# Kernel tuning notes

Measured on AMD Instinct MI355X. Metric: run time of the kernel, lower is better.

Reference implementation:

```python
import jax, jax.numpy as jnp
import numpy as np

# pywt db4 decomposition lowpass filter
DEC_LO = np.array([-0.010597401785069032, 0.0328830116668852, 0.030841381835560764,
                   -0.18703481171909309, -0.027983769416859854, 0.6308807679298589,
                   0.7148465705529157, 0.2303778133088965])
# pytorch_wavelets pre-reverses filters so that torch's cross-correlation conv1d
# implements true convolution; lax.conv_general_dilated is also cross-correlation,
# so we use the same reversed kernel.
KERNEL_LO = jnp.asarray(DEC_LO[::-1].copy(), dtype=jnp.float32)
FLEN = 8


def dwt_lo(x):
    # Single-level db4 lowpass analysis with 'zero' padding, matching
    # pytorch_wavelets afb1d (mode='zero'). x: [B, N, D] -> [B, (N+7)//2, D]
    B, N, D = x.shape
    out = (N + FLEN - 1) // 2            # pywt.dwt_coeff_len(N, 8, 'zero')
    p = 2 * (out - 1) - N + FLEN         # total zero padding
    xr = x.transpose(0, 2, 1).reshape(B * D, 1, N)
    y = jax.lax.conv_general_dilated(xr, KERNEL_LO[None, None, :],
                                     window_strides=(2,),
                                     padding=[(p // 2, p - p // 2)])
    return y.reshape(B, D, out).transpose(0, 2, 1)


def setup_inputs() -> dict:
    key = jax.random.key(0)
    k1, k2 = jax.random.split(key)
    x = jax.random.normal(k1, (32, 4097, 768), dtype=jnp.float32)
    cls_attention_map = jax.random.uniform(k2, (32, 4096), dtype=jnp.float32)
    return {"x": x, "cls_attention_map": cls_attention_map}


def reference(x, cls_attention_map):
    factors = jnp.array([1.5, 0.5], dtype=jnp.float32)  # sorted descending
    B, N, D = x.shape
    cls_tok, patches = x[:, :1], x[:, 1:]

    # per-sample entropy of the CLS attention map
    ent = -jnp.sum(cls_attention_map * jnp.log2(cls_attention_map + 1e-9), axis=-1)  # [B]
    mean, std = ent.mean(), ent.std(ddof=1)  # torch .std() is unbiased
    thr = mean - factors * std               # [2]
    lvl = jnp.sum(ent[:, None] < thr[None, :], axis=1)          # [B]
    lvl = jnp.where(std < 1e-6, jnp.ones_like(lvl), lvl)        # degenerate-std fallback
    lvl = jnp.clip(lvl, 1, factors.shape[0])                    # clamp_min_(1)

    # compute both experts densely, then per-sample select (replaces gather/scatter)
    y1 = dwt_lo(patches)   # level-1 Yl : [B, L1, D], L1 = 2051
    y2 = dwt_lo(y1)        # level-2 Yl : [B, L2, D], L2 = 1029 (cascaded lowpass = J=2 cA)
    L1, L2 = y1.shape[1], y2.shape[1]
    y2p = jnp.pad(y2, ((0, 0), (0, L1 - L2), (0, 0)))

    is1 = (lvl == 1)
    final_patches = jnp.where(is1[:, None, None], y1, y2p)      # [B, L1, D]
    out_len = jnp.where(is1, L1, L2)                            # [B]

    final_x = jnp.concatenate([cls_tok, final_patches], axis=1)  # [B, 1+L1, D]
    mask = jnp.arange(L1)[None, :] < out_len[:, None]
    mask = jnp.concatenate([jnp.ones((B, 1), dtype=bool), mask], axis=1)
    return final_x, mask
```

## Files before the change

### kernel.cpp

```cpp
#include <hip/hip_runtime.h>
#include <hip/hip_bf16.h>
#include <math.h>


typedef float f4 __attribute__((ext_vector_type(4)));

#define B_       32
#define NTOK     4097
#define NPATCH   4096
#define D_       768
#define D4_      192
#define L1_      2051
#define L2_      1029
#define OUTROWS  2052
#define TOUT     16
#define NTILES   129
#define NWG      (B_ * NTILES)

__device__ __constant__ float KLO[8] = {
     0.2303778133088965f,
     0.7148465705529157f,
     0.6308807679298589f,
    -0.027983769416859854f,
    -0.18703481171909309f,
     0.030841381835560764f,
     0.0328830116668852f,
    -0.010597401785069032f
};

__device__ __forceinline__ f4 dot8v(const f4 w[8]) {
    f4 a = KLO[0] * w[0];
#pragma unroll
    for (int t = 1; t < 8; ++t) {
        a.x = fmaf(KLO[t], w[t].x, a.x);
        a.y = fmaf(KLO[t], w[t].y, a.y);
        a.z = fmaf(KLO[t], w[t].z, a.z);
        a.w = fmaf(KLO[t], w[t].w, a.w);
    }
    return a;
}

__global__ void ent_kernel(const float* __restrict__ att, double* __restrict__ ent) {
    __shared__ double sm[256];
    const int b = blockIdx.x;
    const float* a = att + (size_t)b * NPATCH;
    double acc = 0.0;
    for (int i = threadIdx.x; i < NPATCH; i += 256) {
        double v = (double)a[i];
        acc += v * log2(v + 1e-9);
    }
    sm[threadIdx.x] = acc;
    __syncthreads();
    for (int s = 128; s > 0; s >>= 1) {
        if (threadIdx.x < s) sm[threadIdx.x] += sm[threadIdx.x + s];
        __syncthreads();
    }
    if (threadIdx.x == 0) ent[b] = -sm[0];
}

__global__ __launch_bounds__(192) void dwt_kernel(const f4* __restrict__ x,
                                                  const double* __restrict__ ent,
                                                  f4* __restrict__ out,
                                                  float* __restrict__ mask) {
    const int bid  = blockIdx.x;
    const int lid  = (bid & 7) * (NWG / 8) + (bid >> 3);
    const int b    = lid / NTILES;
    const int tile = lid % NTILES;
    const int o0   = tile * TOUT;
    const int d    = threadIdx.x;

    const f4* xb = x + (size_t)b * NTOK * D4_ + d;
    f4* ob = out + (size_t)b * OUTROWS * D4_ + d;

    const f4 z4 = (f4)(0.0f);
    auto xload = [&](int q) -> f4 {
        const int n = q - 6;
        return (n >= 0 && n < NPATCH) ? xb[(size_t)(n + 1) * D4_] : z4;
    };
    auto xrow = [&](int q) -> f4 {
        return xb[(size_t)(q - 5) * D4_];
    };

    const bool interior = (o0 >= TOUT && o0 <= 2016);
    const int q0 = 2 * o0;

    f4 xw[8];
    if (interior) {
#pragma unroll
        for (int t = 0; t < 8; ++t) xw[t] = xrow(q0 + t);
    } else {
#pragma unroll
        for (int t = 0; t < 8; ++t) xw[t] = xload(q0 + t);
    }

    double m = 0.0;
    for (int i = 0; i < B_; ++i) m += ent[i];
    m *= (1.0 / B_);
    double v = 0.0;
    for (int i = 0; i < B_; ++i) { double dd = ent[i] - m; v += dd * dd; }
    v *= (1.0 / (B_ - 1));
    const double sd = sqrt(v);
    const int L = (sd < 1e-6) ? 1 : ((ent[b] < m - 1.5 * sd) ? 2 : 1);

    if (L == 1) {
        if (interior) {
#pragma unroll
            for (int s = 0; s < TOUT; ++s) {
                __builtin_nontemporal_store(dot8v(xw), &ob[(size_t)(o0 + s + 1) * D4_]);
#pragma unroll
                for (int t = 0; t < 6; ++t) xw[t] = xw[t + 2];
                xw[6] = xrow(q0 + 2 * s + 8);
                xw[7] = xrow(q0 + 2 * s + 9);
            }
        } else {
#pragma unroll
            for (int s = 0; s < TOUT; ++s) {
                const int o = o0 + s;
                if (o < L1_) __builtin_nontemporal_store(dot8v(xw), &ob[(size_t)(o + 1) * D4_]);
#pragma unroll
                for (int t = 0; t < 6; ++t) xw[t] = xw[t + 2];
                xw[6] = xload(q0 + 2 * s + 8);
                xw[7] = xload(q0 + 2 * s + 9);
            }
        }
    } else {
        if (o0 >= L2_) {
#pragma unroll
            for (int s = 0; s < TOUT; ++s) {
                const int o = o0 + s;
                if (o < L1_) __builtin_nontemporal_store(z4, &ob[(size_t)(o + 1) * D4_]);
            }
        } else if (o0 >= TOUT && o0 <= 992) {
            int j = 2 * o0 - 6;
#pragma unroll
            for (int t = 0; t < 8; ++t) xw[t] = xrow(2 * j + t);

            auto produceF = [&]() -> f4 {
                f4 vv = dot8v(xw);
#pragma unroll
                for (int t = 0; t < 6; ++t) xw[t] = xw[t + 2];
                xw[6] = xrow(2 * j + 8);
                xw[7] = xrow(2 * j + 9);
                ++j;
                return vv;
            };

            f4 yw[8];
#pragma unroll
            for (int t = 0; t < 8; ++t) yw[t] = produceF();
#pragma unroll
            for (int s = 0; s < TOUT; ++s) {
                __builtin_nontemporal_store(dot8v(yw), &ob[(size_t)(o0 + s + 1) * D4_]);
#pragma unroll
                for (int t = 0; t < 6; ++t) yw[t] = yw[t + 2];
                yw[6] = produceF();
                yw[7] = produceF();
            }
        } else {
            int j = 2 * o0 - 6;
#pragma unroll
            for (int t = 0; t < 8; ++t) xw[t] = xload(2 * j + t);

            auto produce = [&]() -> f4 {
                f4 vv = z4;
                if (j >= 0 && j < L1_) vv = dot8v(xw);
#pragma unroll
                for (int t = 0; t < 6; ++t) xw[t] = xw[t + 2];
                xw[6] = xload(2 * j + 8);
                xw[7] = xload(2 * j + 9);
                ++j;
                return vv;
            };

            f4 yw[8];
#pragma unroll
            for (int t = 0; t < 8; ++t) yw[t] = produce();
#pragma unroll
            for (int s = 0; s < TOUT; ++s) {
                const int o = o0 + s;
                if (o < L1_) {
                    f4 vv = (o < L2_) ? dot8v(yw) : z4;
                    __builtin_nontemporal_store(vv, &ob[(size_t)(o + 1) * D4_]);
                }
#pragma unroll
                for (int t = 0; t < 6; ++t) yw[t] = yw[t + 2];
                yw[6] = produce();
                yw[7] = produce();
            }
        }
    }

    if (tile == 0) ob[0] = xb[0];
    {
        const int len = (L == 1) ? L1_ : L2_;
        const int o = o0 + d;
        if (d < TOUT && o < L1_)
            mask[(size_t)b * OUTROWS + o + 1] = (o < len) ? 1.0f : 0.0f;
        if (tile == 0 && d == TOUT)
            mask[(size_t)b * OUTROWS] = 1.0f;
    }
}

extern "C" void kernel_launch(void* const* d_in, const int* in_sizes, int n_in,
                              void* d_out, int out_size, void* d_ws, size_t ws_size,
                              hipStream_t stream) {
    const float* x   = (const float*)d_in[0];
    const float* att = (const float*)d_in[1];
    float* out  = (float*)d_out;
    float* mask = out + (size_t)B_ * OUTROWS * D_;

    double* ent = (double*)d_ws;

    ent_kernel<<<B_, 256, 0, stream>>>(att, ent);
    dwt_kernel<<<NWG, 192, 0, stream>>>((const f4*)x, ent, (f4*)out, mask);
}
```

Measured before the change: 125.1 us.

## Split workgroups into two row-halves by two column tiles; use fast float log2

Each 192-thread workgroup now handles 32 output rows across half the feature columns (96 f4 lanes), with each half of the threads covering 16 rows, where before one workgroup covered 16 rows across all columns. The number of workgroups stays about the same, but the per-block row span changes the memory access footprint and may affect L2 locality and the overlapping input halo reads. The entropy kernel also switches from double-precision log2 to float __log2f, which cuts expensive FP64 transcendental work but may slightly change entropy values near the level thresholds.

```diff
diff --git a/kernel.cpp b/kernel.cpp
--- a/kernel.cpp
+++ b/kernel.cpp
@@ -14,8 +14,10 @@
 #define L2_      1029
 #define OUTROWS  2052
 #define TOUT     16
-#define NTILES   129
-#define NWG      (B_ * NTILES)
+#define RT       32
+#define NRT      65
+#define NCT      2
+#define NWG      (B_ * NRT * NCT)
 
 __device__ __constant__ float KLO[8] = {
      0.2303778133088965f,
@@ -46,8 +48,8 @@
     const float* a = att + (size_t)b * NPATCH;
     double acc = 0.0;
     for (int i = threadIdx.x; i < NPATCH; i += 256) {
-        double v = (double)a[i];
-        acc += v * log2(v + 1e-9);
+        const float v = a[i];
+        acc += (double)(v * __log2f(v + 1e-9f));
     }
     sm[threadIdx.x] = acc;
     __syncthreads();
@@ -62,15 +64,22 @@
                                                   const double* __restrict__ ent,
                                                   f4* __restrict__ out,
                                                   float* __restrict__ mask) {
-    const int bid  = blockIdx.x;
-    const int lid  = (bid & 7) * (NWG / 8) + (bid >> 3);
-    const int b    = lid / NTILES;
-    const int tile = lid % NTILES;
-    const int o0   = tile * TOUT;
-    const int d    = threadIdx.x;
-
-    const f4* xb = x + (size_t)b * NTOK * D4_ + d;
-    f4* ob = out + (size_t)b * OUTROWS * D4_ + d;
+    const int bid   = blockIdx.x;
+    const int lid   = (bid & 7) * (NWG / 8) + (bid >> 3);
+    const int b     = lid / (NRT * NCT);
+    const int rem   = lid % (NRT * NCT);
+    const int rtile = rem >> 1;
+    const int ctile = rem & 1;
+
+    const int tid  = threadIdx.x;
+    const int half = tid / 96;
+    const int dl   = tid % 96;
+    const int c    = ctile * 96 + dl;
+    const int oB   = rtile * RT + half * TOUT;
+    const int q0   = 2 * oB;
+
+    const f4* xb = x + (size_t)b * NTOK * D4_ + c;
+    f4* ob = out + (size_t)b * OUTROWS * D4_ + c;
 
     const f4 z4 = (f4)(0.0f);
     auto xload = [&](int q) -> f4 {
@@ -81,8 +90,7 @@
         return xb[(size_t)(q - 5) * D4_];
     };
 
-    const bool interior = (o0 >= TOUT && o0 <= 2016);
-    const int q0 = 2 * o0;
+    const bool interior = (oB >= TOUT && oB <= 2016);
 
     f4 xw[8];
     if (interior) {
@@ -106,7 +114,7 @@
         if (interior) {
 #pragma unroll
             for (int s = 0; s < TOUT; ++s) {
-                __builtin_nontemporal_store(dot8v(xw), &ob[(size_t)(o0 + s + 1) * D4_]);
+                __builtin_nontemporal_store(dot8v(xw), &ob[(size_t)(oB + s + 1) * D4_]);
 #pragma unroll
                 for (int t = 0; t < 6; ++t) xw[t] = xw[t + 2];
                 xw[6] = xrow(q0 + 2 * s + 8);
@@ -115,7 +123,7 @@
         } else {
 #pragma unroll
             for (int s = 0; s < TOUT; ++s) {
-                const int o = o0 + s;
+                const int o = oB + s;
                 if (o < L1_) __builtin_nontemporal_store(dot8v(xw), &ob[(size_t)(o + 1) * D4_]);
 #pragma unroll
                 for (int t = 0; t < 6; ++t) xw[t] = xw[t + 2];
@@ -124,14 +132,14 @@
             }
         }
     } else {
-        if (o0 >= L2_) {
-#pragma unroll
-            for (int s = 0; s < TOUT; ++s) {
-                const int o = o0 + s;
+        if (oB >= L2_) {
+#pragma unroll
+            for (int s = 0; s < TOUT; ++s) {
+                const int o = oB + s;
                 if (o < L1_) __builtin_nontemporal_store(z4, &ob[(size_t)(o + 1) * D4_]);
             }
-        } else if (o0 >= TOUT && o0 <= 992) {
-            int j = 2 * o0 - 6;
+        } else if (oB >= TOUT && oB <= 992) {
+            int j = 2 * oB - 6;
 #pragma unroll
             for (int t = 0; t < 8; ++t) xw[t] = xrow(2 * j + t);
 
@@ -150,14 +158,14 @@
             for (int t = 0; t < 8; ++t) yw[t] = produceF();
 #pragma unroll
             for (int s = 0; s < TOUT; ++s) {
-                __builtin_nontemporal_store(dot8v(yw), &ob[(size_t)(o0 + s + 1) * D4_]);
+                __builtin_nontemporal_store(dot8v(yw), &ob[(size_t)(oB + s + 1) * D4_]);
 #pragma unroll
                 for (int t = 0; t < 6; ++t) yw[t] = yw[t + 2];
                 yw[6] = produceF();
                 yw[7] = produceF();
             }
         } else {
-            int j = 2 * o0 - 6;
+            int j = 2 * oB - 6;
 #pragma unroll
             for (int t = 0; t < 8; ++t) xw[t] = xload(2 * j + t);
 
@@ -177,7 +185,7 @@
             for (int t = 0; t < 8; ++t) yw[t] = produce();
 #pragma unroll
             for (int s = 0; s < TOUT; ++s) {
-                const int o = o0 + s;
+                const int o = oB + s;
                 if (o < L1_) {
                     f4 vv = (o < L2_) ? dot8v(yw) : z4;
                     __builtin_nontemporal_store(vv, &ob[(size_t)(o + 1) * D4_]);
@@ -190,13 +198,15 @@
         }
     }
 
-    if (tile == 0) ob[0] = xb[0];
-    {
+    if (rtile == 0 && half == 0) ob[0] = xb[0];
+    if (ctile == 0) {
         const int len = (L == 1) ? L1_ : L2_;
-        const int o = o0 + d;
-        if (d < TOUT && o < L1_)
-            mask[(size_t)b * OUTROWS + o + 1] = (o < len) ? 1.0f : 0.0f;
-        if (tile == 0 && d == TOUT)
+        if (tid < RT) {
+            const int o = rtile * RT + tid;
+            if (o < L1_)
+                mask[(size_t)b * OUTROWS + o + 1] = (o < len) ? 1.0f : 0.0f;
+        }
+        if (rtile == 0 && tid == RT)
             mask[(size_t)b * OUTROWS] = 1.0f;
     }
 }
```

Result: no change. 126.9 us (+1.4%).
